# Optimization experiments

Hardware: AMD Instinct MI355X
Metric: run time of the kernel (lower is better)

## Reference

```python
import jax, jax.numpy as jnp
import numpy as np

C = 16
CO = 16
H = 4
CH = CO // H
CPW = 2 * C


def setup_inputs() -> dict:
    key = jax.random.key(0)
    ks = jax.random.split(key, 12)
    B, N, Nk = 2, 1024, 1024
    s = 0.1
    return {
        "xq": jax.random.normal(ks[0], (B, N, C), jnp.float32),
        "xk": jax.random.normal(ks[1], (B, Nk, C), jnp.float32),
        # fc_w: Linear(2C,2C) -> ReLU -> Linear(2C,H) -> ReLU   (stored as [in,out])
        "w1": jax.random.normal(ks[2], (CPW, CPW), jnp.float32) * s,
        "b1": jax.random.normal(ks[3], (CPW,), jnp.float32) * s,
        "w2": jax.random.normal(ks[4], (CPW, H), jnp.float32) * s,
        "b2": jax.random.normal(ks[5], (H,), jnp.float32) * s,
        # fc_v: Linear(2C,Co) -> ReLU -> Linear(Co,Co) -> ReLU
        "v1": jax.random.normal(ks[6], (CPW, CO), jnp.float32) * s,
        "bv1": jax.random.normal(ks[7], (CO,), jnp.float32) * s,
        "v2": jax.random.normal(ks[8], (CO, CO), jnp.float32) * s,
        "bv2": jax.random.normal(ks[9], (CO,), jnp.float32) * s,
    }


def reference(xq, xk, w1, b1, w2, b2, v1, bv1, v2, bv2):
    B, N, _ = xq.shape
    Nk = xk.shape[1]
    # pad/add/subtract trick in the source reduces to concat(xq, xk - xq)
    diff = xk[:, None, :, :] - xq[:, :, None, :]               # [B,N,Nk,C]
    xq_b = jnp.broadcast_to(xq[:, :, None, :], diff.shape)     # [B,N,Nk,C]
    x_pw = jnp.concatenate([xq_b, diff], axis=-1)              # [B,N,Nk,2C]
    # fc_w -> logits [B,N,Nk,H], softmax over Nk
    hw = jax.nn.relu(x_pw @ w1 + b1)
    logits = jax.nn.relu(hw @ w2 + b2)
    weight = jax.nn.softmax(logits, axis=2)                    # [B,N,Nk,H]
    # fc_v -> value [B,N,Nk,H,Ch]
    hv = jax.nn.relu(x_pw @ v1 + bv1)
    value = jax.nn.relu(hv @ v2 + bv2).reshape(B, N, Nk, H, CH)
    out = jnp.einsum('bnkh,bnkhc->bnhc', weight, value)        # sum over Nk
    return out.reshape(B, N, CO)
```

## Files before the change

kernel.cpp:

```cpp
#include <hip/hip_runtime.h>
#include <hip/hip_bf16.h>
#include <math.h>

static constexpr int Cc   = 16;
static constexpr int COc  = 16;
static constexpr int Hh   = 4;
static constexpr int CPWc = 32;
static constexpr int NTH  = 256;
static constexpr int MTH  = 512;
static constexpr int TFL  = 768;

typedef __attribute__((ext_vector_type(8))) short bf16x8;
typedef __attribute__((ext_vector_type(4))) float f32x4v;

union F4 { float4 v; float f[4]; };

__device__ __forceinline__ short f2bf(float x) {
  __hip_bfloat16 h = __float2bfloat16(x);
  return *reinterpret_cast<short*>(&h);
}

__global__ __launch_bounds__(NTH) void ppa_precompute(
    const float* __restrict__ xq, const float* __restrict__ xk,
    const float* __restrict__ w1, const float* __restrict__ b1,
    const float* __restrict__ v1, const float* __restrict__ bv1,
    const float* __restrict__ w2, const float* __restrict__ v2,
    float* __restrict__ aW, float* __restrict__ aV,
    float* __restrict__ cP,
    ushort* __restrict__ w2f, ushort* __restrict__ v2f,
    int BN, int BK, int Nk, int nRowBlocks) {
  const int t = threadIdx.x;

  if (blockIdx.x == nRowBlocks) {
    if (t < 64) {
      const int n = t & 15, g = t >> 4;
#pragma unroll
      for (int i = 0; i < 8; ++i) {
        const int k = g * 8 + i;
        w2f[t * 8 + i] = (n < Hh) ? (ushort)f2bf(w2[k * Hh + n]) : (ushort)0;
        v2f[t * 8 + i] = (ushort)f2bf(0.5f * v2[(k & 15) * COc + n]);
      }
    }
    return;
  }

  __shared__ float sw1[CPWc * CPWc];
  __shared__ float sv1[CPWc * COc];
  __shared__ float sb1[CPWc];
  __shared__ float sbv1[COc];
  for (int i = t; i < CPWc * CPWc; i += NTH) sw1[i] = w1[i];
  for (int i = t; i < CPWc * COc; i += NTH) sv1[i] = v1[i];
  if (t < CPWc) sb1[t] = b1[t];
  if (t < COc) sbv1[t] = bv1[t];
  __syncthreads();

  const int r = blockIdx.x * 64 + (t >> 2);
  const int sub = t & 3;
  if (r >= BN + BK) return;
  const bool isQ = (r < BN);
  const int rr = isQ ? r : (r - BN);
  const float* src = isQ ? (xq + (size_t)rr * Cc) : (xk + (size_t)rr * Cc);

  float x[Cc];
#pragma unroll
  for (int i = 0; i < Cc; i += 4) {
    float4 v = *reinterpret_cast<const float4*>(src + i);
    x[i] = v.x; x[i + 1] = v.y; x[i + 2] = v.z; x[i + 3] = v.w;
  }

  if (isQ) {
    F4 o0, o1, ov;
#pragma unroll
    for (int jj = 0; jj < 8; ++jj) {
      const int j = sub * 8 + jj;
      float acc = sb1[j];
#pragma unroll
      for (int i = 0; i < Cc; ++i)
        acc += x[i] * (sw1[i * CPWc + j] - sw1[(i + Cc) * CPWc + j]);
      if (jj < 4) o0.f[jj] = acc; else o1.f[jj - 4] = acc;
    }
#pragma unroll
    for (int jj = 0; jj < 4; ++jj) {
      const int j = sub * 4 + jj;
      float acc = sbv1[j];
#pragma unroll
      for (int i = 0; i < Cc; ++i)
        acc += x[i] * (sv1[i * COc + j] - sv1[(i + Cc) * COc + j]);
      ov.f[jj] = acc;
    }
    float* ap = aW + (size_t)rr * CPWc + sub * 8;
    *reinterpret_cast<float4*>(ap) = o0.v;
    *reinterpret_cast<float4*>(ap + 4) = o1.v;
    *reinterpret_cast<float4*>(aV + (size_t)rr * COc + sub * 4) = ov.v;
  } else {
    F4 w0, w1s, cv4;
#pragma unroll
    for (int jj = 0; jj < 8; ++jj) {
      const int j = sub * 8 + jj;
      float acc = 0.f;
#pragma unroll
      for (int i = 0; i < Cc; ++i) acc += x[i] * sw1[(i + Cc) * CPWc + j];
      if (jj < 4) w0.f[jj] = acc; else w1s.f[jj - 4] = acc;
    }
#pragma unroll
    for (int jj = 0; jj < 4; ++jj) {
      const int j = sub * 4 + jj;
      float acc = 0.f;
#pragma unroll
      for (int i = 0; i < Cc; ++i) acc += x[i] * sv1[(i + Cc) * COc + j];
      cv4.f[jj] = acc;
    }
    const int bb = rr / Nk;
    const int kk = rr - bb * Nk;
    const int T = kk >> 4, mm = kk & 15;
    float* tp = cP + ((size_t)bb * (Nk >> 4) + T) * TFL;
    const int g = sub;
    *reinterpret_cast<float4*>(tp + (g * 16 + mm) * 4) = w0.v;
    *reinterpret_cast<float4*>(tp + 256 + (g * 16 + mm) * 4) = w1s.v;
    const int gg = sub >> 1, half = sub & 1;
    *reinterpret_cast<float4*>(tp + 512 + half * 128 + (gg * 16 + mm) * 4) = cv4.v;
  }
}

__global__ __launch_bounds__(MTH) void ppa_main_mfma(
    const float* __restrict__ aW, const float* __restrict__ aV,
    const float* __restrict__ cP,
    const ushort* __restrict__ w2f, const float* __restrict__ b2,
    const ushort* __restrict__ v2f, const float* __restrict__ bv2,
    float* __restrict__ out, int N, int Nk) {
  __shared__ float sro[8][COc];
  __shared__ float srl[8][Hh];

  const int t = threadIdx.x;
  const int lane = t & 63, w = t >> 6;
  const int q = w & 3;
  const int m = lane & 15;
  const int g = lane >> 4;
  const int gg = g & 1;
  const int l31 = lane & 31;
  const int hh = m >> 2;
  const int psrc = (lane & 48) | hh;
  const int row0 = blockIdx.x * 2;
  const int row = row0 + (w >> 2);
  const int b = row0 / N;

  float a_reg[8];
  {
    const float* aRow = aW + (size_t)row * CPWc + g * 8;
#pragma unroll
    for (int i = 0; i < 8; i += 4) {
      F4 v; v.v = *reinterpret_cast<const float4*>(aRow + i);
      a_reg[i] = v.f[0]; a_reg[i + 1] = v.f[1];
      a_reg[i + 2] = v.f[2]; a_reg[i + 3] = v.f[3];
    }
  }
  float av_reg[8];
  {
    const float* avRow = aV + (size_t)row * COc + gg * 8;
#pragma unroll
    for (int i = 0; i < 8; i += 4) {
      F4 v; v.v = *reinterpret_cast<const float4*>(avRow + i);
      av_reg[i] = v.f[0]; av_reg[i + 1] = v.f[1];
      av_reg[i + 2] = v.f[2]; av_reg[i + 3] = v.f[3];
    }
  }
  const bf16x8 wfrag = *reinterpret_cast<const bf16x8*>(w2f + lane * 8);
  const bf16x8 vfrag = *reinterpret_cast<const bf16x8*>(v2f + lane * 8);
  const float b2h = b2[m < Hh ? m : (Hh - 1)];
  const float bv2c = bv2[m];
  const f32x4v cbW = {b2h, b2h, b2h, b2h};
  const f32x4v cbV = {bv2c, bv2c, bv2c, bv2c};

  float o_acc = 0.f, l_acc = 0.f;

  const float* tb = cP + ((size_t)b * (Nk >> 4) + (size_t)q * 16) * TFL;

  F4 c0, c1, d0, d1;
  c0.v = *reinterpret_cast<const float4*>(tb + lane * 4);
  c1.v = *reinterpret_cast<const float4*>(tb + 256 + lane * 4);
  d0.v = *reinterpret_cast<const float4*>(tb + 512 + l31 * 4);
  d1.v = *reinterpret_cast<const float4*>(tb + 640 + l31 * 4);

#pragma unroll
  for (int s = 0; s < 16; ++s) {
    F4 n0 = {}, n1 = {}, e0 = {}, e1 = {};
    if (s < 15) {
      const float* nb = tb + (size_t)(s + 1) * TFL;
      n0.v = *reinterpret_cast<const float4*>(nb + lane * 4);
      n1.v = *reinterpret_cast<const float4*>(nb + 256 + lane * 4);
      e0.v = *reinterpret_cast<const float4*>(nb + 512 + l31 * 4);
      e1.v = *reinterpret_cast<const float4*>(nb + 640 + l31 * 4);
    }

    const bf16x8 afW = {
      f2bf(fmaxf(a_reg[0] + c0.f[0], 0.f)),
      f2bf(fmaxf(a_reg[1] + c0.f[1], 0.f)),
      f2bf(fmaxf(a_reg[2] + c0.f[2], 0.f)),
      f2bf(fmaxf(a_reg[3] + c0.f[3], 0.f)),
      f2bf(fmaxf(a_reg[4] + c1.f[0], 0.f)),
      f2bf(fmaxf(a_reg[5] + c1.f[1], 0.f)),
      f2bf(fmaxf(a_reg[6] + c1.f[2], 0.f)),
      f2bf(fmaxf(a_reg[7] + c1.f[3], 0.f)),
    };
    const f32x4v lgD =
        __builtin_amdgcn_mfma_f32_16x16x32_bf16(afW, wfrag, cbW, 0, 0, 0);

    const float p0 = __expf(fmaxf(lgD[0], 0.f));
    const float p1 = __expf(fmaxf(lgD[1], 0.f));
    const float p2 = __expf(fmaxf(lgD[2], 0.f));
    const float p3 = __expf(fmaxf(lgD[3], 0.f));

    const float q0 = __shfl(p0, psrc);
    const float q1 = __shfl(p1, psrc);
    const float q2 = __shfl(p2, psrc);
    const float q3 = __shfl(p3, psrc);
    if ((m & 3) == 0) l_acc += (q0 + q1) + (q2 + q3);

    const bf16x8 afV = {
      f2bf(fmaxf(av_reg[0] + d0.f[0], 0.f)),
      f2bf(fmaxf(av_reg[1] + d0.f[1], 0.f)),
      f2bf(fmaxf(av_reg[2] + d0.f[2], 0.f)),
      f2bf(fmaxf(av_reg[3] + d0.f[3], 0.f)),
      f2bf(fmaxf(av_reg[4] + d1.f[0], 0.f)),
      f2bf(fmaxf(av_reg[5] + d1.f[1], 0.f)),
      f2bf(fmaxf(av_reg[6] + d1.f[2], 0.f)),
      f2bf(fmaxf(av_reg[7] + d1.f[3], 0.f)),
    };
    const f32x4v vD =
        __builtin_amdgcn_mfma_f32_16x16x32_bf16(afV, vfrag, cbV, 0, 0, 0);

    o_acc += q0 * fmaxf(vD[0], 0.f);
    o_acc += q1 * fmaxf(vD[1], 0.f);
    o_acc += q2 * fmaxf(vD[2], 0.f);
    o_acc += q3 * fmaxf(vD[3], 0.f);

    c0 = n0; c1 = n1; d0 = e0; d1 = e1;
  }

  o_acc += __shfl_xor(o_acc, 16);
  o_acc += __shfl_xor(o_acc, 32);
  l_acc += __shfl_xor(l_acc, 16);
  l_acc += __shfl_xor(l_acc, 32);
  if (lane < COc) sro[w][m] = o_acc;
  if (lane < COc && (lane & 3) == 0) srl[w][lane >> 2] = l_acc;
  __syncthreads();

  if (t < 2 * COc) {
    const int r = t >> 4, c = t & 15, h = c >> 2;
    const int wb = r * 4;
    const float osum = (sro[wb][c] + sro[wb + 1][c]) +
                       (sro[wb + 2][c] + sro[wb + 3][c]);
    const float lsum = (srl[wb][h] + srl[wb + 1][h]) +
                       (srl[wb + 2][h] + srl[wb + 3][h]);
    out[(size_t)(row0 + r) * COc + c] = osum / lsum;
  }
}

extern "C" void kernel_launch(void* const* d_in, const int* in_sizes, int n_in,
                              void* d_out, int out_size, void* d_ws, size_t ws_size,
                              hipStream_t stream) {
  const float* xq  = (const float*)d_in[0];
  const float* xk  = (const float*)d_in[1];
  const float* w1  = (const float*)d_in[2];
  const float* b1  = (const float*)d_in[3];
  const float* w2  = (const float*)d_in[4];
  const float* b2  = (const float*)d_in[5];
  const float* v1  = (const float*)d_in[6];
  const float* bv1 = (const float*)d_in[7];
  const float* v2  = (const float*)d_in[8];
  const float* bv2 = (const float*)d_in[9];
  float* out = (float*)d_out;

  const int BN = in_sizes[0] / Cc;
  const int BK = in_sizes[1] / Cc;
  const int B = 2;
  const int N = BN / B;
  const int Nk = BK / B;

  float* ws = (float*)d_ws;
  float* aW = ws;
  float* aV = aW + (size_t)BN * CPWc;
  float* cP = aV + (size_t)BN * COc;
  ushort* w2f = (ushort*)(cP + (size_t)BK * 48);
  ushort* v2f = w2f + 64 * 8;

  const int totalRows = BN + BK;
  const int nRowBlocks = (totalRows + 63) / 64;
  ppa_precompute<<<nRowBlocks + 1, NTH, 0, stream>>>(
      xq, xk, w1, b1, v1, bv1, w2, v2,
      aW, aV, cP, w2f, v2f, BN, BK, Nk, nRowBlocks);
  ppa_main_mfma<<<BN / 2, MTH, 0, stream>>>(aW, aV, cP, w2f, b2, v2f, bv2,
                                            out, N, Nk);
}
```

Measured before the change: 30.29 us.

## Switch pairwise MFMA path to fp16 with packed relu and replicated head weights

Stores the key-side precomputed tile in fp16 instead of fp32, halving the per-iteration global loads, and does the bias add and ReLU with packed half2 math before feeding f16 MFMAs. The w2 fragment is replicated across the four columns of each head, so each lane already holds its head's logit and the per-step shuffles are removed. This lowers precision of the hidden activations (fp16 range and rounding versus bf16 and fp32 adds) and changes the tile layout consistently in producer and consumer.

```diff
diff --git a/kernel.cpp b/kernel.cpp
--- a/kernel.cpp
+++ b/kernel.cpp
@@ -8,16 +8,27 @@
 static constexpr int CPWc = 32;
 static constexpr int NTH  = 256;
 static constexpr int MTH  = 512;
-static constexpr int TFL  = 768;
-
-typedef __attribute__((ext_vector_type(8))) short bf16x8;
+static constexpr int TFH  = 768;
+
+typedef _Float16 f16x2 __attribute__((ext_vector_type(2)));
+typedef _Float16 f16x8 __attribute__((ext_vector_type(8)));
 typedef __attribute__((ext_vector_type(4))) float f32x4v;
 
 union F4 { float4 v; float f[4]; };
-
-__device__ __forceinline__ short f2bf(float x) {
-  __hip_bfloat16 h = __float2bfloat16(x);
-  return *reinterpret_cast<short*>(&h);
+union H8 {
+  f16x8 v8;
+  struct { f16x2 q0, q1, q2, q3; } p;
+  float4 f4;
+};
+
+__device__ __forceinline__ ushort f2h(float x) {
+  _Float16 h = (_Float16)x;
+  ushort u;
+  __builtin_memcpy(&u, &h, 2);
+  return u;
+}
+__device__ __forceinline__ f16x2 relu2(f16x2 x) {
+  return __builtin_elementwise_max(x, (f16x2)(_Float16)0);
 }
 
 __global__ __launch_bounds__(NTH) void ppa_precompute(
@@ -26,7 +37,7 @@
     const float* __restrict__ v1, const float* __restrict__ bv1,
     const float* __restrict__ w2, const float* __restrict__ v2,
     float* __restrict__ aW, float* __restrict__ aV,
-    float* __restrict__ cP,
+    ushort* __restrict__ cP,
     ushort* __restrict__ w2f, ushort* __restrict__ v2f,
     int BN, int BK, int Nk, int nRowBlocks) {
   const int t = threadIdx.x;
@@ -37,8 +48,8 @@
 #pragma unroll
       for (int i = 0; i < 8; ++i) {
         const int k = g * 8 + i;
-        w2f[t * 8 + i] = (n < Hh) ? (ushort)f2bf(w2[k * Hh + n]) : (ushort)0;
-        v2f[t * 8 + i] = (ushort)f2bf(0.5f * v2[(k & 15) * COc + n]);
+        w2f[t * 8 + i] = f2h(w2[k * Hh + (n >> 2)]);
+        v2f[t * 8 + i] = f2h(0.5f * v2[(k & 15) * COc + n]);
       }
     }
     return;
@@ -93,14 +104,15 @@
     *reinterpret_cast<float4*>(ap + 4) = o1.v;
     *reinterpret_cast<float4*>(aV + (size_t)rr * COc + sub * 4) = ov.v;
   } else {
-    F4 w0, w1s, cv4;
+    float cw[8];
+    float cv4[4];
 #pragma unroll
     for (int jj = 0; jj < 8; ++jj) {
       const int j = sub * 8 + jj;
       float acc = 0.f;
 #pragma unroll
       for (int i = 0; i < Cc; ++i) acc += x[i] * sw1[(i + Cc) * CPWc + j];
-      if (jj < 4) w0.f[jj] = acc; else w1s.f[jj - 4] = acc;
+      cw[jj] = acc;
     }
 #pragma unroll
     for (int jj = 0; jj < 4; ++jj) {
@@ -108,23 +120,28 @@
       float acc = 0.f;
 #pragma unroll
       for (int i = 0; i < Cc; ++i) acc += x[i] * sv1[(i + Cc) * COc + j];
-      cv4.f[jj] = acc;
+      cv4[jj] = acc;
     }
     const int bb = rr / Nk;
     const int kk = rr - bb * Nk;
     const int T = kk >> 4, mm = kk & 15;
-    float* tp = cP + ((size_t)bb * (Nk >> 4) + T) * TFL;
-    const int g = sub;
-    *reinterpret_cast<float4*>(tp + (g * 16 + mm) * 4) = w0.v;
-    *reinterpret_cast<float4*>(tp + 256 + (g * 16 + mm) * 4) = w1s.v;
+    ushort* tp = cP + ((size_t)bb * (Nk >> 4) + T) * TFH;
+    ushort4 h0, h1;
+    h0.x = f2h(cw[0]); h0.y = f2h(cw[1]); h0.z = f2h(cw[2]); h0.w = f2h(cw[3]);
+    h1.x = f2h(cw[4]); h1.y = f2h(cw[5]); h1.z = f2h(cw[6]); h1.w = f2h(cw[7]);
+    ushort* wp = tp + (sub * 16 + mm) * 8;
+    *reinterpret_cast<ushort4*>(wp) = h0;
+    *reinterpret_cast<ushort4*>(wp + 4) = h1;
+    ushort4 hv;
+    hv.x = f2h(cv4[0]); hv.y = f2h(cv4[1]); hv.z = f2h(cv4[2]); hv.w = f2h(cv4[3]);
     const int gg = sub >> 1, half = sub & 1;
-    *reinterpret_cast<float4*>(tp + 512 + half * 128 + (gg * 16 + mm) * 4) = cv4.v;
+    *reinterpret_cast<ushort4*>(tp + 512 + (gg * 16 + mm) * 8 + half * 4) = hv;
   }
 }
 
 __global__ __launch_bounds__(MTH) void ppa_main_mfma(
     const float* __restrict__ aW, const float* __restrict__ aV,
-    const float* __restrict__ cP,
+    const ushort* __restrict__ cP,
     const ushort* __restrict__ w2f, const float* __restrict__ b2,
     const ushort* __restrict__ v2f, const float* __restrict__ bv2,
     float* __restrict__ out, int N, int Nk) {
@@ -139,102 +156,83 @@
   const int gg = g & 1;
   const int l31 = lane & 31;
   const int hh = m >> 2;
-  const int psrc = (lane & 48) | hh;
   const int row0 = blockIdx.x * 2;
   const int row = row0 + (w >> 2);
   const int b = row0 / N;
 
-  float a_reg[8];
+  f16x2 a01, a23, a45, a67, av01, av23, av45, av67;
   {
     const float* aRow = aW + (size_t)row * CPWc + g * 8;
-#pragma unroll
-    for (int i = 0; i < 8; i += 4) {
-      F4 v; v.v = *reinterpret_cast<const float4*>(aRow + i);
-      a_reg[i] = v.f[0]; a_reg[i + 1] = v.f[1];
-      a_reg[i + 2] = v.f[2]; a_reg[i + 3] = v.f[3];
-    }
-  }
-  float av_reg[8];
-  {
+    F4 v0, v1;
+    v0.v = *reinterpret_cast<const float4*>(aRow);
+    v1.v = *reinterpret_cast<const float4*>(aRow + 4);
+    a01 = f16x2{(_Float16)v0.f[0], (_Float16)v0.f[1]};
+    a23 = f16x2{(_Float16)v0.f[2], (_Float16)v0.f[3]};
+    a45 = f16x2{(_Float16)v1.f[0], (_Float16)v1.f[1]};
+    a67 = f16x2{(_Float16)v1.f[2], (_Float16)v1.f[3]};
     const float* avRow = aV + (size_t)row * COc + gg * 8;
-#pragma unroll
-    for (int i = 0; i < 8; i += 4) {
-      F4 v; v.v = *reinterpret_cast<const float4*>(avRow + i);
-      av_reg[i] = v.f[0]; av_reg[i + 1] = v.f[1];
-      av_reg[i + 2] = v.f[2]; av_reg[i + 3] = v.f[3];
-    }
-  }
-  const bf16x8 wfrag = *reinterpret_cast<const bf16x8*>(w2f + lane * 8);
-  const bf16x8 vfrag = *reinterpret_cast<const bf16x8*>(v2f + lane * 8);
-  const float b2h = b2[m < Hh ? m : (Hh - 1)];
+    F4 u0, u1;
+    u0.v = *reinterpret_cast<const float4*>(avRow);
+    u1.v = *reinterpret_cast<const float4*>(avRow + 4);
+    av01 = f16x2{(_Float16)u0.f[0], (_Float16)u0.f[1]};
+    av23 = f16x2{(_Float16)u0.f[2], (_Float16)u0.f[3]};
+    av45 = f16x2{(_Float16)u1.f[0], (_Float16)u1.f[1]};
+    av67 = f16x2{(_Float16)u1.f[2], (_Float16)u1.f[3]};
+  }
+  const f16x8 wfrag = *reinterpret_cast<const f16x8*>(w2f + lane * 8);
+  const f16x8 vfrag = *reinterpret_cast<const f16x8*>(v2f + lane * 8);
+  const float b2h = b2[hh];
   const float bv2c = bv2[m];
   const f32x4v cbW = {b2h, b2h, b2h, b2h};
   const f32x4v cbV = {bv2c, bv2c, bv2c, bv2c};
 
   float o_acc = 0.f, l_acc = 0.f;
 
-  const float* tb = cP + ((size_t)b * (Nk >> 4) + (size_t)q * 16) * TFL;
-
-  F4 c0, c1, d0, d1;
-  c0.v = *reinterpret_cast<const float4*>(tb + lane * 4);
-  c1.v = *reinterpret_cast<const float4*>(tb + 256 + lane * 4);
-  d0.v = *reinterpret_cast<const float4*>(tb + 512 + l31 * 4);
-  d1.v = *reinterpret_cast<const float4*>(tb + 640 + l31 * 4);
+  const ushort* tb = cP + ((size_t)b * (Nk >> 4) + (size_t)q * 16) * TFH;
+
+  H8 cw, cv;
+  cw.f4 = *reinterpret_cast<const float4*>(tb + lane * 8);
+  cv.f4 = *reinterpret_cast<const float4*>(tb + 512 + l31 * 8);
 
 #pragma unroll
   for (int s = 0; s < 16; ++s) {
-    F4 n0 = {}, n1 = {}, e0 = {}, e1 = {};
+    H8 nw, nv;
+    nw.f4 = float4{0.f, 0.f, 0.f, 0.f};
+    nv.f4 = float4{0.f, 0.f, 0.f, 0.f};
     if (s < 15) {
-      const float* nb = tb + (size_t)(s + 1) * TFL;
-      n0.v = *reinterpret_cast<const float4*>(nb + lane * 4);
-      n1.v = *reinterpret_cast<const float4*>(nb + 256 + lane * 4);
-      e0.v = *reinterpret_cast<const float4*>(nb + 512 + l31 * 4);
-      e1.v = *reinterpret_cast<const float4*>(nb + 640 + l31 * 4);
-    }
-
-    const bf16x8 afW = {
-      f2bf(fmaxf(a_reg[0] + c0.f[0], 0.f)),
-      f2bf(fmaxf(a_reg[1] + c0.f[1], 0.f)),
-      f2bf(fmaxf(a_reg[2] + c0.f[2], 0.f)),
-      f2bf(fmaxf(a_reg[3] + c0.f[3], 0.f)),
-      f2bf(fmaxf(a_reg[4] + c1.f[0], 0.f)),
-      f2bf(fmaxf(a_reg[5] + c1.f[1], 0.f)),
-      f2bf(fmaxf(a_reg[6] + c1.f[2], 0.f)),
-      f2bf(fmaxf(a_reg[7] + c1.f[3], 0.f)),
-    };
+      const ushort* nb = tb + (size_t)(s + 1) * TFH;
+      nw.f4 = *reinterpret_cast<const float4*>(nb + lane * 8);
+      nv.f4 = *reinterpret_cast<const float4*>(nb + 512 + l31 * 8);
+    }
+
+    H8 fw;
+    fw.p.q0 = relu2(a01 + cw.p.q0);
+    fw.p.q1 = relu2(a23 + cw.p.q1);
+    fw.p.q2 = relu2(a45 + cw.p.q2);
+    fw.p.q3 = relu2(a67 + cw.p.q3);
     const f32x4v lgD =
-        __builtin_amdgcn_mfma_f32_16x16x32_bf16(afW, wfrag, cbW, 0, 0, 0);
+        __builtin_amdgcn_mfma_f32_16x16x32_f16(fw.v8, wfrag, cbW, 0, 0, 0);
 
     const float p0 = __expf(fmaxf(lgD[0], 0.f));
     const float p1 = __expf(fmaxf(lgD[1], 0.f));
     const float p2 = __expf(fmaxf(lgD[2], 0.f));
     const float p3 = __expf(fmaxf(lgD[3], 0.f));
-
-    const float q0 = __shfl(p0, psrc);
-    const float q1 = __shfl(p1, psrc);
-    const float q2 = __shfl(p2, psrc);
-    const float q3 = __shfl(p3, psrc);
-    if ((m & 3) == 0) l_acc += (q0 + q1) + (q2 + q3);
-
-    const bf16x8 afV = {
-      f2bf(fmaxf(av_reg[0] + d0.f[0], 0.f)),
-      f2bf(fmaxf(av_reg[1] + d0.f[1], 0.f)),
-      f2bf(fmaxf(av_reg[2] + d0.f[2], 0.f)),
-      f2bf(fmaxf(av_reg[3] + d0.f[3], 0.f)),
-      f2bf(fmaxf(av_reg[4] + d1.f[0], 0.f)),
-      f2bf(fmaxf(av_reg[5] + d1.f[1], 0.f)),
-      f2bf(fmaxf(av_reg[6] + d1.f[2], 0.f)),
-      f2bf(fmaxf(av_reg[7] + d1.f[3], 0.f)),
-    };
+    if ((m & 3) == 0) l_acc += (p0 + p1) + (p2 + p3);
+
+    H8 fv;
+    fv.p.q0 = relu2(av01 + cv.p.q0);
+    fv.p.q1 = relu2(av23 + cv.p.q1);
+    fv.p.q2 = relu2(av45 + cv.p.q2);
+    fv.p.q3 = relu2(av67 + cv.p.q3);
     const f32x4v vD =
-        __builtin_amdgcn_mfma_f32_16x16x32_bf16(afV, vfrag, cbV, 0, 0, 0);
-
-    o_acc += q0 * fmaxf(vD[0], 0.f);
-    o_acc += q1 * fmaxf(vD[1], 0.f);
-    o_acc += q2 * fmaxf(vD[2], 0.f);
-    o_acc += q3 * fmaxf(vD[3], 0.f);
-
-    c0 = n0; c1 = n1; d0 = e0; d1 = e1;
+        __builtin_amdgcn_mfma_f32_16x16x32_f16(fv.v8, vfrag, cbV, 0, 0, 0);
+
+    o_acc += p0 * fmaxf(vD[0], 0.f);
+    o_acc += p1 * fmaxf(vD[1], 0.f);
+    o_acc += p2 * fmaxf(vD[2], 0.f);
+    o_acc += p3 * fmaxf(vD[3], 0.f);
+
+    cw = nw; cv = nv;
   }
 
   o_acc += __shfl_xor(o_acc, 16);
@@ -280,8 +278,8 @@
   float* ws = (float*)d_ws;
   float* aW = ws;
   float* aV = aW + (size_t)BN * CPWc;
-  float* cP = aV + (size_t)BN * COc;
-  ushort* w2f = (ushort*)(cP + (size_t)BK * 48);
+  ushort* cP = (ushort*)(aV + (size_t)BN * COc);
+  ushort* w2f = cP + (size_t)BK * 48;
   ushort* v2f = w2f + 64 * 8;
 
   const int totalRows = BN + BK;
```

Measured after the change: 25.72 us. 15.1% less time.
